# Performance work log

Measured on AMD Instinct MI355X. Metric: run time of the kernel, lower is better.

## Reference

```python
import jax, jax.numpy as jnp
import numpy as np

B, T, V, E, U = 64, 256, 128, 512, 512


def _lstm_scan(zx, mask_t, Ur, reverse):
    """Masked LSTM over time-major precomputed input projections.
    zx: [T,B,4U] = x@W + b; mask_t: [T,B] bool; Ur: [U,4U].
    Masked steps carry previous h,c (Keras mask semantics).
    reverse=True implements the backward direction of Bidirectional
    (lax.scan reverse keeps outputs aligned with input time order,
    matching Keras' go_backwards + output re-reversal).
    """
    u = Ur.shape[0]
    b = zx.shape[1]

    def step(carry, inp):
        h, c = carry
        zx_t, m = inp
        z = zx_t + h @ Ur
        i, f, g, o = jnp.split(z, 4, axis=-1)
        i = jax.nn.sigmoid(i)
        f = jax.nn.sigmoid(f)
        g = jnp.tanh(g)
        o = jax.nn.sigmoid(o)
        c_new = f * c + i * g
        h_new = o * jnp.tanh(c_new)
        m = m[:, None]
        h_new = jnp.where(m, h_new, h)
        c_new = jnp.where(m, c_new, c)
        return (h_new, c_new), h_new

    init = (jnp.zeros((b, u), zx.dtype), jnp.zeros((b, u), zx.dtype))
    (h, c), ys = jax.lax.scan(step, init, (zx, mask_t), reverse=reverse)
    return ys, h, c


def _bidir_lstm(x, mask_t, Wf, Uf, bf, Wb, Ub, bb):
    # x: [B,T,D] -> time-major [T,B,D]
    xt = jnp.transpose(x, (1, 0, 2))
    ysf, hf, cf = _lstm_scan(xt @ Wf + bf, mask_t, Uf, False)
    ysb, hb, cb = _lstm_scan(xt @ Wb + bb, mask_t, Ub, True)
    ys = jnp.concatenate([ysf, ysb], axis=-1)  # [T,B,2U]
    return (jnp.transpose(ys, (1, 0, 2)),
            jnp.concatenate([hf, hb], axis=-1),
            jnp.concatenate([cf, cb], axis=-1))


def _lstm_params(key, in_dim, units):
    k1, k2, k3 = jax.random.split(key, 3)
    W = jax.random.normal(k1, (in_dim, 4 * units), jnp.float32) / np.sqrt(in_dim)
    Ur = jax.random.normal(k2, (units, 4 * units), jnp.float32) / np.sqrt(units)
    b = jnp.zeros((4 * units,), jnp.float32).at[units:2 * units].set(1.0)  # unit forget bias
    return W, Ur, b


def setup_inputs() -> dict:
    key = jax.random.key(0)
    ks = jax.random.split(key, 6)
    encoder_input = jax.random.randint(ks[0], (B, T), 0, V, dtype=jnp.int32)
    emb = jax.random.normal(ks[1], (V, E), jnp.float32) * 0.05
    W1f, U1f, b1f = _lstm_params(ks[2], E, U)
    W1b, U1b, b1b = _lstm_params(ks[3], E, U)
    W2f, U2f, b2f = _lstm_params(ks[4], 2 * U, U)
    W2b, U2b, b2b = _lstm_params(ks[5], 2 * U, U)
    return {"encoder_input": encoder_input, "emb": emb,
            "W1f": W1f, "U1f": U1f, "b1f": b1f,
            "W1b": W1b, "U1b": U1b, "b1b": b1b,
            "W2f": W2f, "U2f": U2f, "b2f": b2f,
            "W2b": W2b, "U2b": U2b, "b2b": b2b}


def reference(encoder_input, emb, W1f, U1f, b1f, W1b, U1b, b1b,
              W2f, U2f, b2f, W2b, U2b, b2b):
    mask = encoder_input != 0           # [B,T] from mask_zero=True
    mask_t = mask.T                     # [T,B]
    x = emb[encoder_input]              # [B,T,E]
    out1, _h1, _c1 = _bidir_lstm(x, mask_t, W1f, U1f, b1f, W1b, U1b, b1b)
    # dropout is identity at inference (training=False)
    out2, h2, c2 = _bidir_lstm(out1, mask_t, W2f, U2f, b2f, W2b, U2b, b2b)
    return out2, h2, c2
```

## Files before the change

kernel.cpp:

```cpp
#include <hip/hip_runtime.h>

typedef unsigned short u16;
typedef unsigned int u32;
typedef unsigned long long u64;
typedef __attribute__((ext_vector_type(8))) short bf16x8;
typedef __attribute__((ext_vector_type(4))) float f32x4;
typedef __attribute__((ext_vector_type(8))) unsigned short u16x8;
typedef __attribute__((ext_vector_type(4))) unsigned short u16x4;

#define MFMA16(a, b, c) __builtin_amdgcn_mfma_f32_16x16x32_bf16(a, b, c, 0, 0, 0)

__device__ __forceinline__ u16 f2b(float f) {
    u32 u = __builtin_bit_cast(u32, f);
    u32 r = (u + 0x7fffu + ((u >> 16) & 1u)) >> 16;
    return (u16)r;
}
__device__ __forceinline__ float b2f(u16 h) {
    u32 u = ((u32)h) << 16;
    return __builtin_bit_cast(float, u);
}
__device__ __forceinline__ float sigm(float x) { return 1.0f / (1.0f + __expf(-x)); }
__device__ __forceinline__ float tanh_fast(float x) { return 1.0f - 2.0f / (__expf(2.0f * x) + 1.0f); }

__device__ __forceinline__ u32 aload32(const void* p) {
    return __hip_atomic_load((const u32*)p, __ATOMIC_RELAXED, __HIP_MEMORY_SCOPE_AGENT);
}
__device__ __forceinline__ void astore32(void* p, u32 v) {
    __hip_atomic_store((u32*)p, v, __ATOMIC_RELAXED, __HIP_MEMORY_SCOPE_AGENT);
}
__device__ __forceinline__ void astore64(void* p, u64 v) {
    __hip_atomic_store((u64*)p, v, __ATOMIC_RELAXED, __HIP_MEMORY_SCOPE_AGENT);
}

__global__ __launch_bounds__(256) void embed_k(const int* __restrict__ enc,
                                               const float* __restrict__ emb,
                                               u16* __restrict__ xb) {
    int idx = (blockIdx.x * 256 + threadIdx.x) * 4;
    int row = idx >> 9;
    int e = idx & 511;
    int t = row >> 6, b = row & 63;
    int tok = enc[b * 256 + t];
    const float4 v = *(const float4*)(emb + (size_t)tok * 512 + e);
    u16x4 o;
    o.x = f2b(v.x); o.y = f2b(v.y); o.z = f2b(v.z); o.w = f2b(v.w);
    *(u16x4*)(xb + idx) = o;
}

__global__ void mask_k(const int* __restrict__ enc, u64* __restrict__ mw) {
    int t = threadIdx.x;
    u64 m = 0;
#pragma unroll 8
    for (int b = 0; b < 64; ++b)
        if (enc[b * 256 + t] != 0) m |= (1ull << b);
    mw[t] = m;
}

__global__ __launch_bounds__(256) void castT_k(const float* __restrict__ src,
                                               u16* __restrict__ dst, int K, int N) {
    __shared__ float tile[64][65];
    int n0 = blockIdx.x * 64, k0 = blockIdx.y * 64;
    int tid = threadIdx.x;
#pragma unroll
    for (int it = 0; it < 4; ++it) {
        int e = tid + it * 256;
        int kk = e >> 4;
        int nn = (e & 15) * 4;
        const float4 v = *(const float4*)(src + (size_t)(k0 + kk) * N + n0 + nn);
        tile[kk][nn] = v.x; tile[kk][nn + 1] = v.y;
        tile[kk][nn + 2] = v.z; tile[kk][nn + 3] = v.w;
    }
    __syncthreads();
#pragma unroll
    for (int it = 0; it < 2; ++it) {
        int e = tid + it * 256;
        int nn = e >> 3;
        int ks = (e & 7) * 8;
        u16x8 o;
#pragma unroll
        for (int j = 0; j < 8; ++j) o[j] = f2b(tile[ks + j][nn]);
        *(u16x8*)(dst + (size_t)(n0 + nn) * K + k0 + ks) = o;
    }
}

__global__ __launch_bounds__(256) void gemm_bias_k(
    const u16* __restrict__ A, int Ak,
    const u16* __restrict__ BtF, const u16* __restrict__ BtB,
    const float* __restrict__ biasF, const float* __restrict__ biasB,
    u16* __restrict__ outF, u16* __restrict__ outB) {
    const int dir = blockIdx.z;
    const u16* __restrict__ Bt = dir ? BtB : BtF;
    const float* __restrict__ bias = dir ? biasB : biasF;
    u16* __restrict__ out = dir ? outB : outF;

    const int m0 = blockIdx.y * 128, n0 = blockIdx.x * 128;
    __shared__ __align__(16) u16 As[128 * 40];
    __shared__ __align__(16) u16 Bs[128 * 40];
    const int tid = threadIdx.x;
    const int lane = tid & 63, w = tid >> 6;
    const int l15 = lane & 15, quad = lane >> 4;
    const int rb = (w >> 1) * 64, cb = (w & 1) * 64;

    f32x4 acc[4][4];
#pragma unroll
    for (int i = 0; i < 4; ++i)
#pragma unroll
        for (int j = 0; j < 4; ++j) acc[i][j] = (f32x4){0.f, 0.f, 0.f, 0.f};

    const int nkt = Ak >> 5;
    for (int kt = 0; kt < nkt; ++kt) {
        __syncthreads();
#pragma unroll
        for (int it = 0; it < 2; ++it) {
            int s = tid + it * 256;
            int r = s >> 2, seg = s & 3;
            *(uint4*)&As[r * 40 + seg * 8] =
                *(const uint4*)&A[(size_t)(m0 + r) * Ak + kt * 32 + seg * 8];
            *(uint4*)&Bs[r * 40 + seg * 8] =
                *(const uint4*)&Bt[(size_t)(n0 + r) * Ak + kt * 32 + seg * 8];
        }
        __syncthreads();
        bf16x8 af[4], bfr[4];
#pragma unroll
        for (int i = 0; i < 4; ++i)
            af[i] = *(const bf16x8*)&As[(rb + i * 16 + l15) * 40 + quad * 8];
#pragma unroll
        for (int j = 0; j < 4; ++j)
            bfr[j] = *(const bf16x8*)&Bs[(cb + j * 16 + l15) * 40 + quad * 8];
#pragma unroll
        for (int i = 0; i < 4; ++i)
#pragma unroll
            for (int j = 0; j < 4; ++j) acc[i][j] = MFMA16(af[i], bfr[j], acc[i][j]);
    }
#pragma unroll
    for (int j = 0; j < 4; ++j) {
        int col = n0 + cb + j * 16 + l15;
        float bv = bias[col];
#pragma unroll
        for (int i = 0; i < 4; ++i) {
            int m = m0 + rb + i * 16 + quad * 4;
            int t = m >> 6, b0 = m & 63;
            int grp = b0 >> 4, bi = b0 & 15;
            u16x4 o;
#pragma unroll
            for (int r = 0; r < 4; ++r) o[r] = f2b(acc[i][j][r] + bv);
            *(u16x4*)&out[(((size_t)t * 4 + grp) * 2048 + col) * 16 + bi] = o;
        }
    }
}

__global__ __launch_bounds__(256, 1) void lstm_rec_k(
    const u16* __restrict__ zxF, const u16* __restrict__ zxB,
    const u16* __restrict__ UtF, const u16* __restrict__ UtB,
    const u64* __restrict__ maskw,
    u16* __restrict__ hex,
    u32* __restrict__ flgs,
    float* __restrict__ out2,
    int layer) {
    const int wg = blockIdx.x;
    const int dir = wg >> 6;
    const int grp = (wg >> 4) & 3;
    const int wu = wg & 15;
    const u16* __restrict__ zx = dir ? zxB : zxF;
    const u16* __restrict__ Ut = dir ? UtB : UtF;
    u32* __restrict__ flg = flgs + (dir * 4 + grp) * 32;

    const int tid = threadIdx.x;
    const int lane = tid & 63, w = tid >> 6;
    const int l15 = lane & 15, quad = lane >> 4;
    const bool hi = (lane & 8) != 0;
    const int gc_l = (l15 >> 3) * 512 + wu * 32 + w * 8 + (l15 & 7);
    const int u = wu * 32 + w * 8 + (lane & 7);
    const int brow = grp * 16 + l15;
    const int b0 = grp * 16 + quad * 4;
    const int bi0 = quad * 4;

    bf16x8 bfr[2][16];
#pragma unroll
    for (int nt = 0; nt < 2; ++nt)
#pragma unroll
        for (int kt = 0; kt < 16; ++kt)
            bfr[nt][kt] = *(const bf16x8*)&Ut[(size_t)(nt * 1024 + gc_l) * 512 + kt * 32 + quad * 8];

    float hreg[4] = {0.f, 0.f, 0.f, 0.f};
    float creg[4] = {0.f, 0.f, 0.f, 0.f};

    int t0 = dir ? 255 : 0;
    u16x4 pz0 = *(const u16x4*)&zx[(((size_t)t0 * 4 + grp) * 2048 + gc_l) * 16 + bi0];
    u16x4 pz1 = *(const u16x4*)&zx[(((size_t)t0 * 4 + grp) * 2048 + 1024 + gc_l) * 16 + bi0];

    for (int s = 0; s < 256; ++s) {
        const int t = dir ? (255 - s) : s;
        const int tp = dir ? (t + 1) : (t - 1);

        if (s) {
            if (tid < 16) {
                u32 v = aload32(&flg[tid]);
                while (__ballot(v < (u32)s)) v = aload32(&flg[tid]);
            }
            __syncthreads();
        }

        const u64 mw = maskw[t];

        f32x4 acc0, acc1;
#pragma unroll
        for (int r = 0; r < 4; ++r) { acc0[r] = b2f(pz0[r]); acc1[r] = b2f(pz1[r]); }

        if (s) {
            const u16* hbase = hex + ((size_t)tp * 64 + brow) * 1024 + dir * 512 + quad * 8;
            bf16x8 hfr[16];
#pragma unroll
            for (int kt = 0; kt < 16; ++kt) hfr[kt] = *(const bf16x8*)&hbase[kt * 32];
#pragma unroll
            for (int kt = 0; kt < 16; ++kt) {
                acc0 = MFMA16(hfr[kt], bfr[0][kt], acc0);
                acc1 = MFMA16(hfr[kt], bfr[1][kt], acc1);
            }
        }

#pragma unroll
        for (int r = 0; r < 4; ++r) {
            int b = b0 + r;
            float z0 = acc0[r], z1 = acc1[r];
            float p0 = __shfl_xor(z0, 8);
            float p1 = __shfl_xor(z1, 8);
            float iz = hi ? p0 : z0, fz = hi ? z0 : p0;
            float gz = hi ? p1 : z1, oz = hi ? z1 : p1;
            float i_ = sigm(iz), f_ = sigm(fz), g_ = tanh_fast(gz), o_ = sigm(oz);
            float cn = f_ * creg[r] + i_ * g_;
            float hv = o_ * tanh_fast(cn);
            if (!((mw >> b) & 1ull)) { cn = creg[r]; hv = hreg[r]; }
            creg[r] = cn; hreg[r] = hv;
            if (!hi) {
                u16 hb = f2b(hv);
                u32 pair = (u32)hb | (((u32)(u16)__shfl_xor((int)(u32)hb, 1)) << 16);
                u64 q = (u64)pair | ((u64)(u32)__shfl_xor((int)pair, 2) << 32);
                if (!(lane & 3))
                    astore64(&hex[((size_t)t * 64 + b) * 1024 + dir * 512 + u], q);
            }
        }

        __syncthreads();
        if (tid == 0) astore32(&flg[wu], (u32)(s + 1));

        if (layer == 2 && !hi) {
#pragma unroll
            for (int r = 0; r < 4; ++r) {
                u32 h32 = __builtin_bit_cast(u32, hreg[r]);
                u32 ot = (u32)__shfl_xor((int)h32, 1);
                if (!(lane & 1)) {
                    u64 qq = (u64)h32 | ((u64)ot << 32);
                    *(u64*)&out2[(size_t)(b0 + r) * 262144 + (size_t)t * 1024 + dir * 512 + u] = qq;
                }
            }
            if (s == 255) {
#pragma unroll
                for (int r = 0; r < 4; ++r) {
                    int b = b0 + r;
                    out2[16777216 + b * 1024 + dir * 512 + u] = hreg[r];
                    out2[16777216 + 65536 + b * 1024 + dir * 512 + u] = creg[r];
                }
            }
        }
        {
            int tn = dir ? (s < 255 ? 254 - s : 0) : (s < 255 ? s + 1 : 255);
            pz0 = *(const u16x4*)&zx[(((size_t)tn * 4 + grp) * 2048 + gc_l) * 16 + bi0];
            pz1 = *(const u16x4*)&zx[(((size_t)tn * 4 + grp) * 2048 + 1024 + gc_l) * 16 + bi0];
        }
    }
}

extern "C" void kernel_launch(void* const* d_in, const int* in_sizes, int n_in,
                              void* d_out, int out_size, void* d_ws, size_t ws_size,
                              hipStream_t stream) {
    const int* enc = (const int*)d_in[0];
    const float* emb = (const float*)d_in[1];
    const float* W1f = (const float*)d_in[2];
    const float* U1f = (const float*)d_in[3];
    const float* b1f = (const float*)d_in[4];
    const float* W1b = (const float*)d_in[5];
    const float* U1b = (const float*)d_in[6];
    const float* b1b = (const float*)d_in[7];
    const float* W2f = (const float*)d_in[8];
    const float* U2f = (const float*)d_in[9];
    const float* b2f = (const float*)d_in[10];
    const float* W2b = (const float*)d_in[11];
    const float* U2b = (const float*)d_in[12];
    const float* b2b = (const float*)d_in[13];

    char* ws = (char*)d_ws;
    constexpr size_t ZXF = 0;
    constexpr size_t ZXB = 67108864;
    constexpr size_t XB = 134217728;
    constexpr size_t OUT1 = 150994944;
    constexpr size_t WT = 184549376;
    constexpr size_t W1FT = WT + 0;
    constexpr size_t W1BT = WT + 2097152;
    constexpr size_t U1FT = WT + 4194304;
    constexpr size_t U1BT = WT + 6291456;
    constexpr size_t W2FT = WT + 8388608;
    constexpr size_t W2BT = WT + 12582912;
    constexpr size_t U2FT = WT + 16777216;
    constexpr size_t U2BT = WT + 18874368;
    constexpr size_t FLG = 205520896;
    constexpr size_t MASKW = FLG + 4096;

    u16* zxF = (u16*)(ws + ZXF);
    u16* zxB = (u16*)(ws + ZXB);
    u16* xb = (u16*)(ws + XB);
    u16* out1 = (u16*)(ws + OUT1);
    u32* flgs = (u32*)(ws + FLG);
    u64* maskw = (u64*)(ws + MASKW);

    hipMemsetAsync(ws + FLG, 0, 4096, stream);

    embed_k<<<8192, 256, 0, stream>>>(enc, emb, xb);
    mask_k<<<1, 256, 0, stream>>>(enc, maskw);

    castT_k<<<dim3(32, 8), 256, 0, stream>>>(W1f, (u16*)(ws + W1FT), 512, 2048);
    castT_k<<<dim3(32, 8), 256, 0, stream>>>(W1b, (u16*)(ws + W1BT), 512, 2048);
    castT_k<<<dim3(32, 8), 256, 0, stream>>>(U1f, (u16*)(ws + U1FT), 512, 2048);
    castT_k<<<dim3(32, 8), 256, 0, stream>>>(U1b, (u16*)(ws + U1BT), 512, 2048);
    castT_k<<<dim3(32, 16), 256, 0, stream>>>(W2f, (u16*)(ws + W2FT), 1024, 2048);
    castT_k<<<dim3(32, 16), 256, 0, stream>>>(W2b, (u16*)(ws + W2BT), 1024, 2048);
    castT_k<<<dim3(32, 8), 256, 0, stream>>>(U2f, (u16*)(ws + U2FT), 512, 2048);
    castT_k<<<dim3(32, 8), 256, 0, stream>>>(U2b, (u16*)(ws + U2BT), 512, 2048);

    gemm_bias_k<<<dim3(16, 128, 2), 256, 0, stream>>>(
        xb, 512, (u16*)(ws + W1FT), (u16*)(ws + W1BT), b1f, b1b, zxF, zxB);
    lstm_rec_k<<<128, 256, 0, stream>>>(
        zxF, zxB, (u16*)(ws + U1FT), (u16*)(ws + U1BT), maskw,
        out1, flgs, nullptr, 1);

    gemm_bias_k<<<dim3(16, 128, 2), 256, 0, stream>>>(
        out1, 1024, (u16*)(ws + W2FT), (u16*)(ws + W2BT), b2f, b2b, zxF, zxB);
    hipMemsetAsync(ws + FLG, 0, 4096, stream);
    lstm_rec_k<<<128, 256, 0, stream>>>(
        zxF, zxB, (u16*)(ws + U2FT), (u16*)(ws + U2BT), maskw,
        out1, flgs, (float*)d_out, 2);
}
```

Before: 2.857 ms.

## Replace flag-based step barrier with sentinel-filled hidden-state polling

Removes the per-step flag counters and the two __syncthreads around them in the persistent LSTM recurrence kernel. The hidden-state exchange buffer is pre-filled with 0xFF, and each consumer polls its 64-bit h chunks with atomic loads until none equals the all-ones sentinel. The intent is to cut the critical-path latency of the cross-workgroup handoff at each timestep. In exchange it adds two 32 MB memsets. Correctness relies on all-ones never being a valid packed bf16 value and on the 64-bit stores being atomic.

```diff
diff --git a/kernel.cpp b/kernel.cpp
--- a/kernel.cpp
+++ b/kernel.cpp
@@ -22,11 +22,8 @@
 __device__ __forceinline__ float sigm(float x) { return 1.0f / (1.0f + __expf(-x)); }
 __device__ __forceinline__ float tanh_fast(float x) { return 1.0f - 2.0f / (__expf(2.0f * x) + 1.0f); }
 
-__device__ __forceinline__ u32 aload32(const void* p) {
-    return __hip_atomic_load((const u32*)p, __ATOMIC_RELAXED, __HIP_MEMORY_SCOPE_AGENT);
-}
-__device__ __forceinline__ void astore32(void* p, u32 v) {
-    __hip_atomic_store((u32*)p, v, __ATOMIC_RELAXED, __HIP_MEMORY_SCOPE_AGENT);
+__device__ __forceinline__ u64 aload64(const void* p) {
+    return __hip_atomic_load((const u64*)p, __ATOMIC_RELAXED, __HIP_MEMORY_SCOPE_AGENT);
 }
 __device__ __forceinline__ void astore64(void* p, u64 v) {
     __hip_atomic_store((u64*)p, v, __ATOMIC_RELAXED, __HIP_MEMORY_SCOPE_AGENT);
@@ -153,7 +150,6 @@
     const u16* __restrict__ UtF, const u16* __restrict__ UtB,
     const u64* __restrict__ maskw,
     u16* __restrict__ hex,
-    u32* __restrict__ flgs,
     float* __restrict__ out2,
     int layer) {
     const int wg = blockIdx.x;
@@ -162,17 +158,16 @@
     const int wu = wg & 15;
     const u16* __restrict__ zx = dir ? zxB : zxF;
     const u16* __restrict__ Ut = dir ? UtB : UtF;
-    u32* __restrict__ flg = flgs + (dir * 4 + grp) * 32;
 
     const int tid = threadIdx.x;
     const int lane = tid & 63, w = tid >> 6;
     const int l15 = lane & 15, quad = lane >> 4;
     const bool hi = (lane & 8) != 0;
     const int gc_l = (l15 >> 3) * 512 + wu * 32 + w * 8 + (l15 & 7);
-    const int u = wu * 32 + w * 8 + (lane & 7);
     const int brow = grp * 16 + l15;
     const int b0 = grp * 16 + quad * 4;
     const int bi0 = quad * 4;
+    const int u = wu * 32 + w * 8 + (lane & 7);
 
     bf16x8 bfr[2][16];
 #pragma unroll
@@ -188,18 +183,12 @@
     u16x4 pz0 = *(const u16x4*)&zx[(((size_t)t0 * 4 + grp) * 2048 + gc_l) * 16 + bi0];
     u16x4 pz1 = *(const u16x4*)&zx[(((size_t)t0 * 4 + grp) * 2048 + 1024 + gc_l) * 16 + bi0];
 
+    union HU { u64 q[2]; bf16x8 v; };
+
     for (int s = 0; s < 256; ++s) {
         const int t = dir ? (255 - s) : s;
         const int tp = dir ? (t + 1) : (t - 1);
 
-        if (s) {
-            if (tid < 16) {
-                u32 v = aload32(&flg[tid]);
-                while (__ballot(v < (u32)s)) v = aload32(&flg[tid]);
-            }
-            __syncthreads();
-        }
-
         const u64 mw = maskw[t];
 
         f32x4 acc0, acc1;
@@ -208,13 +197,28 @@
 
         if (s) {
             const u16* hbase = hex + ((size_t)tp * 64 + brow) * 1024 + dir * 512 + quad * 8;
-            bf16x8 hfr[16];
-#pragma unroll
-            for (int kt = 0; kt < 16; ++kt) hfr[kt] = *(const bf16x8*)&hbase[kt * 32];
+            HU hu[16];
+            u32 inval = 0xffffu;
+            while (true) {
+#pragma unroll
+                for (int kt = 0; kt < 16; ++kt)
+                    if (inval & (1u << kt)) {
+                        hu[kt].q[0] = aload64(hbase + kt * 32);
+                        hu[kt].q[1] = aload64(hbase + kt * 32 + 4);
+                    }
+                u32 ni = 0;
+#pragma unroll
+                for (int kt = 0; kt < 16; ++kt)
+                    if ((inval & (1u << kt)) &&
+                        (hu[kt].q[0] == ~0ull || hu[kt].q[1] == ~0ull))
+                        ni |= 1u << kt;
+                inval = ni;
+                if (!__ballot(inval != 0u)) break;
+            }
 #pragma unroll
             for (int kt = 0; kt < 16; ++kt) {
-                acc0 = MFMA16(hfr[kt], bfr[0][kt], acc0);
-                acc1 = MFMA16(hfr[kt], bfr[1][kt], acc1);
+                acc0 = MFMA16(hu[kt].v, bfr[0][kt], acc0);
+                acc1 = MFMA16(hu[kt].v, bfr[1][kt], acc1);
             }
         }
 
@@ -240,9 +244,6 @@
             }
         }
 
-        __syncthreads();
-        if (tid == 0) astore32(&flg[wu], (u32)(s + 1));
-
         if (layer == 2 && !hi) {
 #pragma unroll
             for (int r = 0; r < 4; ++r) {
@@ -302,17 +303,15 @@
     constexpr size_t W2BT = WT + 12582912;
     constexpr size_t U2FT = WT + 16777216;
     constexpr size_t U2BT = WT + 18874368;
-    constexpr size_t FLG = 205520896;
-    constexpr size_t MASKW = FLG + 4096;
+    constexpr size_t MASKW = 205520896 + 4096;
 
     u16* zxF = (u16*)(ws + ZXF);
     u16* zxB = (u16*)(ws + ZXB);
     u16* xb = (u16*)(ws + XB);
     u16* out1 = (u16*)(ws + OUT1);
-    u32* flgs = (u32*)(ws + FLG);
     u64* maskw = (u64*)(ws + MASKW);
 
-    hipMemsetAsync(ws + FLG, 0, 4096, stream);
+    hipMemsetAsync(ws + OUT1, 0xFF, 33554432, stream);
 
     embed_k<<<8192, 256, 0, stream>>>(enc, emb, xb);
     mask_k<<<1, 256, 0, stream>>>(enc, maskw);
@@ -330,12 +329,12 @@
         xb, 512, (u16*)(ws + W1FT), (u16*)(ws + W1BT), b1f, b1b, zxF, zxB);
     lstm_rec_k<<<128, 256, 0, stream>>>(
         zxF, zxB, (u16*)(ws + U1FT), (u16*)(ws + U1BT), maskw,
-        out1, flgs, nullptr, 1);
+        out1, nullptr, 1);
 
     gemm_bias_k<<<dim3(16, 128, 2), 256, 0, stream>>>(
         out1, 1024, (u16*)(ws + W2FT), (u16*)(ws + W2BT), b2f, b2b, zxF, zxB);
-    hipMemsetAsync(ws + FLG, 0, 4096, stream);
+    hipMemsetAsync(ws + OUT1, 0xFF, 33554432, stream);
     lstm_rec_k<<<128, 256, 0, stream>>>(
         zxF, zxB, (u16*)(ws + U2FT), (u16*)(ws + U2BT), maskw,
-        out1, flgs, (float*)d_out, 2);
-}
+        out1, (float*)d_out, 2);
+}
```

After: 3.744 ms. 31.0% more time.
